# Performance work log

Measured on AMD Instinct MI355X. Metric: run time of the kernel, lower is better.

Reference implementation:

```python
import jax, jax.numpy as jnp
import numpy as np
from math import factorial

# module hyperparameters (match init_kwargs)
IN_FEATURES = 512
TAU_0 = 0.1
DT = 0.1
K = 4
C = 0.1
ALPHA = 1.0
G = 0
NTAU = 400
T_EVERY = 4
SEQ = 512


def _build_constants():
    """Replicates _calc_tau_star / _calc_D / _calc_invL in float64 numpy."""
    n = NTAU + 2 * K  # 408
    tau_star = TAU_0 * (1.0 + C) ** np.arange(-K, NTAU + K, dtype=np.float64)
    s = K / tau_star
    s0 = s[1:-1] - s[:-2]
    s1 = s[2:] - s[1:-1]
    s11 = s[2:] - s[:-2]
    A = -(s1 / s11 / s0)
    B = -(s0 / s11 / s1) + s1 / s11 / s0
    Cc = s0 / s11 / s1
    D = np.zeros((n, n), dtype=np.float64)
    r = np.arange(n - 2)
    D[r + 1, r] = A
    D[r + 1, r + 1] = B
    D[r + 1, r + 2] = Cc
    D = D.T
    invL = ((-1.0) ** K / factorial(K)
            * (np.linalg.matrix_power(D, K) @ np.diag(s ** (K + 1.0))))[:, K:-K].T  # [ntau, n]
    e_alph_dt = np.exp(-s * ALPHA * DT)
    decay = (1.0 / (ALPHA * s)) * (1.0 - e_alph_dt)          # [n]
    d = e_alph_dt ** (TAU_0 / DT)                             # per-step decay (dur = tau_0)
    subset = tau_star[K:-K:T_EVERY] ** G                      # [O]
    invL_sub = invL[::T_EVERY]                                # [O, n] (slice commutes with matmul rows)
    return invL_sub, d, decay, subset


def setup_inputs() -> dict:
    key = jax.random.key(0)
    invL_sub, d, decay, subset = _build_constants()
    inp = jax.random.normal(key, (SEQ, IN_FEATURES), dtype=jnp.float32)
    return {
        "inp": inp,
        "invL_sub": jnp.asarray(invL_sub, jnp.float32),
        "d": jnp.asarray(d, jnp.float32),
        "decay": jnp.asarray(decay, jnp.float32),
        "subset": jnp.asarray(subset, jnp.float32),
    }


def reference(inp, invL_sub, d, decay, subset):
    # t_{c} = diag(e^{-s*alpha*dt})^{dur/dt} t_{c-1} + decay * alpha * inp_c * (dur/dt)
    scale = TAU_0 / DT  # dur/dt with dur defaulting to tau_0
    u = (decay * ALPHA * scale)[None, :, None] * inp[:, None, :]  # [T, n, F]

    def step(t, u_t):
        t_new = d[:, None] * t + u_t
        return t_new, t_new

    t0 = jnp.zeros((d.shape[0], inp.shape[1]), inp.dtype)
    _, ts = jax.lax.scan(step, t0, u)  # [T, n, F]
    # output[c] = (invL @ t_c)[::T_every] * subset_tau_star  (invL rows pre-sliced)
    out = jnp.einsum('on,tnf->tof', invL_sub, ts) * subset[None, :, None]
    return out
```

## Files before the change

### kernel.cpp

```cpp
#include <hip/hip_runtime.h>


#define NF   512
#define NN   408
#define NO   100
#define NC   16
#define TC   32
#define NB   15
#define TAPS 9
#define OPG  5
#define NG   20
#define ROWS 25
#define NPT  4

__global__ __launch_bounds__(256) void sith_pass1(
    const float* __restrict__ inp, const float* __restrict__ d,
    float* __restrict__ P)
{
    int fs = blockIdx.x;
    int a  = blockIdx.y;
    int tid = threadIdx.x;
    int lane = tid & 63;
    int y = tid >> 6;
    int n0 = a * 16 + y * NPT;
    if (n0 >= NN) return;
    int f = fs * 64 + lane;

    float dreg[NPT], st[NPT];
    #pragma unroll
    for (int q = 0; q < NPT; ++q) {
        dreg[q] = d[n0 + q];
        st[q] = 0.f;
    }

    const float* ip = inp + f;
    for (int b = 0; b < NB; ++b) {
        #pragma unroll
        for (int tt = 0; tt < TC; tt += 8) {
            float x[8];
            #pragma unroll
            for (int u = 0; u < 8; ++u)
                x[u] = ip[(b * TC + tt + u) * NF];
            #pragma unroll
            for (int u = 0; u < 8; ++u) {
                #pragma unroll
                for (int q = 0; q < NPT; ++q)
                    st[q] = fmaf(dreg[q], st[q], x[u]);
            }
        }
        #pragma unroll
        for (int q = 0; q < NPT; ++q)
            P[b * (NN * NF) + (n0 + q) * NF + f] = st[q];
    }
}

__global__ __launch_bounds__(256) void sith_pass2(
    const float* __restrict__ inp, const float* __restrict__ invL,
    const float* __restrict__ d, const float* __restrict__ decay,
    const float* __restrict__ subset, const float* __restrict__ P,
    float* __restrict__ out)
{
    int bx = blockIdx.x;
    int fs = bx & 7;
    int oc = bx >> 3;
    int c  = blockIdx.y;
    int tid = threadIdx.x;
    int lane = tid & 63;
    int w = tid >> 6;
    int g = oc * 4 + w;
    int f = fs * 64 + lane;
    int nbase = NG * g;

    float dreg[ROWS], p[ROWS];
    #pragma unroll
    for (int j = 0; j < ROWS; ++j) {
        int n = nbase + j;
        dreg[j] = d[n];
        p[j] = (c == 0) ? 0.f : P[(c - 1) * (NN * NF) + n * NF + f];
    }

    float L[OPG][TAPS];
    #pragma unroll
    for (int k = 0; k < OPG; ++k) {
        int o = OPG * g + k;
        float sub = subset[o];
        #pragma unroll
        for (int dd = 0; dd < TAPS; ++dd) {
            int n = nbase + 4 * k + dd;
            L[k][dd] = invL[o * NN + n] * sub * decay[n];
        }
    }

    const float* ip = inp + f;
    int t0 = c * TC;
    int obase = (t0 * NO + OPG * g) * NF + f;

#define SITH_STEP(xv)                                                      \
    {                                                                      \
        _Pragma("unroll")                                                  \
        for (int j = 0; j < ROWS; ++j)                                     \
            p[j] = fmaf(dreg[j], p[j], (xv));                              \
        _Pragma("unroll")                                                  \
        for (int k = 0; k < OPG; ++k) {                                    \
            float acc = 0.f;                                               \
            _Pragma("unroll")                                              \
            for (int dd = 0; dd < TAPS; ++dd)                              \
                acc = fmaf(L[k][dd], p[4 * k + dd], acc);                  \
            __builtin_nontemporal_store(acc, &out[obase + k * NF]);        \
        }                                                                  \
        obase += NO * NF;                                                  \
    }

    float xb0 = ip[(t0 + 0) * NF];
    float xb1 = ip[(t0 + 1) * NF];
    float xb2 = ip[(t0 + 2) * NF];
    float xb3 = ip[(t0 + 3) * NF];

    for (int tq = 0; tq < TC; tq += 4) {
        int tp = t0 + tq + 4;
        float xn0 = ip[((tp + 0) & 511) * NF];
        float xn1 = ip[((tp + 1) & 511) * NF];
        float xn2 = ip[((tp + 2) & 511) * NF];
        float xn3 = ip[((tp + 3) & 511) * NF];
        SITH_STEP(xb0);
        SITH_STEP(xb1);
        SITH_STEP(xb2);
        SITH_STEP(xb3);
        xb0 = xn0; xb1 = xn1; xb2 = xn2; xb3 = xn3;
    }
#undef SITH_STEP
}

extern "C" void kernel_launch(void* const* d_in, const int* in_sizes, int n_in,
                              void* d_out, int out_size, void* d_ws, size_t ws_size,
                              hipStream_t stream)
{
    const float* inp    = (const float*)d_in[0];
    const float* invL   = (const float*)d_in[1];
    const float* d      = (const float*)d_in[2];
    const float* decay  = (const float*)d_in[3];
    const float* subset = (const float*)d_in[4];
    float* out = (float*)d_out;
    float* P   = (float*)d_ws;

    sith_pass1<<<dim3(8, 26), 256, 0, stream>>>(inp, d, P);
    sith_pass2<<<dim3(40, NC), 256, 0, stream>>>(inp, invL, d, decay, subset, P, out);
}
```

Measured before the change: 39.06 us.

## Parallelize chunk-state pass across chunks and combine prefixes in pass two

Pass 1 used to scan all 15 chunks serially in each thread to produce the carried-in state for every chunk. It now launches one block per chunk along a third grid dimension, and each block computes only that chunk's local zero-start state. Pass 2 rebuilds the carry-in state by folding the local chunk states with d^32 decay factors, so pass 1 no longer has a long serial dependency chain. The cost is extra global reads in pass 2 (up to c-1 chunk states per row), which fall most heavily on later chunks, and repeated squaring of d may change rounding slightly.

```diff
diff --git a/kernel.cpp b/kernel.cpp
--- a/kernel.cpp
+++ b/kernel.cpp
@@ -19,6 +19,7 @@
 {
     int fs = blockIdx.x;
     int a  = blockIdx.y;
+    int b  = blockIdx.z;
     int tid = threadIdx.x;
     int lane = tid & 63;
     int y = tid >> 6;
@@ -33,25 +34,23 @@
         st[q] = 0.f;
     }
 
-    const float* ip = inp + f;
-    for (int b = 0; b < NB; ++b) {
+    const float* ip = inp + b * TC * NF + f;
+    #pragma unroll
+    for (int tt = 0; tt < TC; tt += 8) {
+        float x[8];
         #pragma unroll
-        for (int tt = 0; tt < TC; tt += 8) {
-            float x[8];
+        for (int u = 0; u < 8; ++u)
+            x[u] = ip[(tt + u) * NF];
+        #pragma unroll
+        for (int u = 0; u < 8; ++u) {
             #pragma unroll
-            for (int u = 0; u < 8; ++u)
-                x[u] = ip[(b * TC + tt + u) * NF];
-            #pragma unroll
-            for (int u = 0; u < 8; ++u) {
-                #pragma unroll
-                for (int q = 0; q < NPT; ++q)
-                    st[q] = fmaf(dreg[q], st[q], x[u]);
-            }
+            for (int q = 0; q < NPT; ++q)
+                st[q] = fmaf(dreg[q], st[q], x[u]);
         }
-        #pragma unroll
-        for (int q = 0; q < NPT; ++q)
-            P[b * (NN * NF) + (n0 + q) * NF + f] = st[q];
     }
+    #pragma unroll
+    for (int q = 0; q < NPT; ++q)
+        P[b * (NN * NF) + (n0 + q) * NF + f] = st[q];
 }
 
 __global__ __launch_bounds__(256) void sith_pass2(
@@ -73,10 +72,30 @@
 
     float dreg[ROWS], p[ROWS];
     #pragma unroll
-    for (int j = 0; j < ROWS; ++j) {
-        int n = nbase + j;
-        dreg[j] = d[n];
-        p[j] = (c == 0) ? 0.f : P[(c - 1) * (NN * NF) + n * NF + f];
+    for (int j = 0; j < ROWS; ++j)
+        dreg[j] = d[nbase + j];
+
+    if (c == 0) {
+        #pragma unroll
+        for (int j = 0; j < ROWS; ++j) p[j] = 0.f;
+    } else {
+        float d32[ROWS];
+        #pragma unroll
+        for (int j = 0; j < ROWS; ++j) {
+            float d2 = dreg[j] * dreg[j];
+            float d4 = d2 * d2, d8 = d4 * d4, d16 = d8 * d8;
+            d32[j] = d16 * d16;
+        }
+        const float* Pb = P + nbase * NF + f;
+        #pragma unroll
+        for (int j = 0; j < ROWS; ++j)
+            p[j] = Pb[j * NF];
+        for (int k = 1; k < c; ++k) {
+            const float* Pk = Pb + k * (NN * NF);
+            #pragma unroll
+            for (int j = 0; j < ROWS; ++j)
+                p[j] = fmaf(d32[j], p[j], Pk[j * NF]);
+        }
     }
 
     float L[OPG][TAPS];
@@ -143,6 +162,6 @@
     float* out = (float*)d_out;
     float* P   = (float*)d_ws;
 
-    sith_pass1<<<dim3(8, 26), 256, 0, stream>>>(inp, d, P);
+    sith_pass1<<<dim3(8, 26, NB), 256, 0, stream>>>(inp, d, P);
     sith_pass2<<<dim3(40, NC), 256, 0, stream>>>(inp, invL, d, decay, subset, P, out);
 }
```

After: 36.50 us. -6.5%, faster.
